# Kernel optimization log

Hardware: AMD Instinct MI355X
Metric: run time of the kernel (lower is better)

The kernel has to match this reference:

```python
import jax, jax.numpy as jnp
import numpy as np

B, S, D = 32, 512, 512      # batch, seq, feature
E, H, O, K = 8, 2048, 512, 2  # experts, expert hidden, expert out, top_k


def setup_inputs() -> dict:
    key = jax.random.key(0)
    ks = jax.random.split(key, 5)
    sc = lambda k, shape, scale: jax.random.normal(k, shape, jnp.float32) * scale
    return {
        "x": sc(ks[0], (B, S, D), 1.0),
        "attn_w": sc(ks[1], (D, 1), 0.05),
        "attn_b": jnp.zeros((1,), jnp.float32),
        "gate_w": sc(ks[2], (D, E), 0.05),
        "gate_b": jnp.zeros((E,), jnp.float32),
        "w1": sc(ks[3], (E, D, H), 0.02),
        "b1": jnp.zeros((E, H), jnp.float32),
        "w2": sc(ks[4], (E, H, O), 0.02),
        "b2": jnp.zeros((E, O), jnp.float32),
    }


def reference(x, attn_w, attn_b, gate_w, gate_b, w1, b1, w2, b2):
    # --- attention pooling over the sequence axis ---
    scores = x @ attn_w + attn_b                      # [B,S,1]
    aw = jax.nn.softmax(scores, axis=1)               # softmax over seq
    pooled = jnp.sum(x * aw, axis=1)                  # [B,D]

    # --- gating: softmax -> top-k mask -> renormalize ---
    gates = jax.nn.softmax(pooled @ gate_w + gate_b, axis=-1)  # [B,E]
    _, idx = jax.lax.top_k(gates, K)                  # [B,K]
    mask = jnp.sum(jax.nn.one_hot(idx, E, dtype=gates.dtype), axis=-2)  # [B,E]
    g = gates * mask
    g = g / (jnp.sum(g, axis=-1, keepdims=True) + 1e-9)        # [B,E]

    # --- dense all-experts compute (exact GELU, as keras Dense('gelu')) ---
    h = jax.nn.gelu(jnp.einsum('bsd,edh->ebsh', x, w1) + b1[:, None, None, :],
                    approximate=False)                 # [E,B,S,H]
    eo = jax.nn.gelu(jnp.einsum('ebsh,eho->ebso', h, w2) + b2[:, None, None, :],
                     approximate=False)                # [E,B,S,O]

    # --- weighted combine over experts ---
    return jnp.einsum('ebso,be->bso', eo, g)           # [B,S,O]
```

## Files before the change

kernel.cpp:

```cpp
#include <hip/hip_runtime.h>
#include <hip/hip_bf16.h>
#include <math.h>

#define B_  32
#define S_  512
#define D_  512
#define E_  8
#define H_  2048
#define O_  512

typedef __bf16 bf16x8 __attribute__((ext_vector_type(8)));
typedef float  f32x4  __attribute__((ext_vector_type(4)));

#define GL2LDS(src, dst) \
  __builtin_amdgcn_global_load_lds((const __attribute__((address_space(1))) void*)(src), \
                                   (__attribute__((address_space(3))) void*)(dst), 16, 0, 0)

#define MFMA16(a, b, c) __builtin_amdgcn_mfma_f32_16x16x32_bf16((a), (b), (c), 0, 0, 0)

__device__ __forceinline__ float gelu_fast(float v) {
  float w = v * fmaf(v * v, 0.0713548162f, 1.5957691216f);
  float e = __expf(-w);
  return v * __builtin_amdgcn_rcpf(1.0f + e);
}


__global__ __launch_bounds__(256) void cast_score_kernel(
    const float* __restrict__ x, const float* __restrict__ attn_w,
    char* __restrict__ xpack, float* __restrict__ scores)
{
  const int t = threadIdx.x;
  const int r = t >> 5;
  const int cg = t & 31;
  const int row = blockIdx.x * 8 + r;
  const int bb = row >> 9, s = row & 511;
  const float* src  = x + (size_t)row * D_ + cg * 16;
  const float* wsrc = attn_w + cg * 16;
  char* xp = xpack + (size_t)bb * 524288 + s * 64;
  const int sx = (s >> 1) & 3;
  float acc = 0.f;
#pragma unroll
  for (int k = 0; k < 4; ++k) {
    const int d0 = cg * 16 + k * 4;
    float4 v  = *(const float4*)(src + k * 4);
    float4 wv = *(const float4*)(wsrc + k * 4);
    acc += v.x * wv.x + v.y * wv.y + v.z * wv.z + v.w * wv.w;
    ushort4 o;
    o.x = __builtin_bit_cast(unsigned short, __float2bfloat16(v.x));
    o.y = __builtin_bit_cast(unsigned short, __float2bfloat16(v.y));
    o.z = __builtin_bit_cast(unsigned short, __float2bfloat16(v.z));
    o.w = __builtin_bit_cast(unsigned short, __float2bfloat16(v.w));
    const int u = d0 >> 5;
    const int byte = u * 32768 + ((((d0 >> 3) & 3) ^ sx) << 4) + (d0 & 7) * 2;
    *(ushort4*)(xp + byte) = o;
  }
#pragma unroll
  for (int off = 16; off; off >>= 1) acc += __shfl_xor(acc, off);
  if (cg == 0) scores[row] = acc;
}

__global__ __launch_bounds__(512) void softmax_aw_kernel(
    const float* __restrict__ scores, float* __restrict__ aw)
{
  __shared__ float red[8];
  __shared__ float mm, ss;
  const int t = threadIdx.x, b = blockIdx.x;
  float v = scores[b * S_ + t];
  float m = v;
#pragma unroll
  for (int off = 32; off; off >>= 1) m = fmaxf(m, __shfl_xor(m, off));
  if ((t & 63) == 0) red[t >> 6] = m;
  __syncthreads();
  if (t == 0) {
    float a = red[0];
    for (int i = 1; i < 8; ++i) a = fmaxf(a, red[i]);
    mm = a;
  }
  __syncthreads();
  float e = expf(v - mm);
  float s = e;
#pragma unroll
  for (int off = 32; off; off >>= 1) s += __shfl_xor(s, off);
  if ((t & 63) == 0) red[t >> 6] = s;
  __syncthreads();
  if (t == 0) {
    float a = 0.f;
    for (int i = 0; i < 8; ++i) a += red[i];
    ss = 1.f / a;
  }
  __syncthreads();
  aw[b * S_ + t] = e * ss;
}

__global__ __launch_bounds__(512) void pool_kernel(
    const float* __restrict__ x, const float* __restrict__ aw, float* __restrict__ pooled)
{
  __shared__ float sm[4][128];
  const int t = threadIdx.x;
  const int dl = t & 127;
  const int sh = t >> 7;
  const int b = blockIdx.y;
  const int d = blockIdx.x * 128 + dl;
  const float* xp  = x + (size_t)b * S_ * D_ + d;
  const float* awb = aw + b * S_;
  float acc = 0.f;
#pragma unroll 4
  for (int s = sh; s < S_; s += 4)
    acc = fmaf(awb[s], xp[(size_t)s * D_], acc);
  if (sh) sm[sh][dl] = acc;
  __syncthreads();
  if (sh == 0) pooled[b * D_ + d] = acc + sm[1][dl] + sm[2][dl] + sm[3][dl];
}

__global__ __launch_bounds__(256) void gate_psort_kernel(
    const float* __restrict__ pooled, const float* __restrict__ gate_w,
    const float* __restrict__ gate_b, int* __restrict__ gidx, float* __restrict__ gwt,
    int* __restrict__ psort)
{
  __shared__ float gl[32][8];
  const int t = threadIdx.x;
  const int b = t >> 3, ee = t & 7;
  float z = gate_b[ee];
  const float* pb = pooled + b * D_;
  for (int d = 0; d < D_; ++d) z = fmaf(pb[d], gate_w[d * E_ + ee], z);
  gl[b][ee] = z;
  __syncthreads();
  if (t < 32) {
    float ge[8];
    float zmax = gl[t][0];
    for (int i = 1; i < 8; ++i) zmax = fmaxf(zmax, gl[t][i]);
    float zs = 0.f;
    for (int i = 0; i < 8; ++i) { ge[i] = expf(gl[t][i] - zmax); zs += ge[i]; }
    for (int i = 0; i < 8; ++i) ge[i] /= zs;
    int i0 = 0;
    for (int i = 1; i < 8; ++i) if (ge[i] > ge[i0]) i0 = i;
    int i1 = -1;
    for (int i = 0; i < 8; ++i) if (i != i0 && (i1 < 0 || ge[i] > ge[i1])) i1 = i;
    float denom = ge[i0] + ge[i1] + 1e-9f;
    gidx[t * 2 + 0] = i0; gidx[t * 2 + 1] = i1;
    gwt[t * 2 + 0] = ge[i0] / denom; gwt[t * 2 + 1] = ge[i1] / denom;
  }
  __syncthreads();
  if (t == 0) {
    int cnt[E_] = {}, pos[E_];
    for (int p = 0; p < 2 * B_; ++p) cnt[gidx[p]]++;
    int s = 0;
    for (int e2 = 0; e2 < E_; ++e2) { pos[e2] = s; s += cnt[e2]; }
    for (int p = 0; p < 2 * B_; ++p) psort[pos[gidx[p]]++] = p;
  }
}

__global__ void pack_w_kernel(const float* __restrict__ in, char* __restrict__ outp,
                              int R, int C)
{
  __shared__ float tile[32][33];
  const int z = blockIdx.z;
  const float* inz = in + (size_t)z * R * C;
  const int c0 = blockIdx.x * 32, r0 = blockIdx.y * 32;
  const int tx = threadIdx.x, ty = threadIdx.y;
#pragma unroll
  for (int jj = 0; jj < 4; ++jj) {
    int r = r0 + ty + jj * 8;
    tile[ty + jj * 8][tx] = inz[(size_t)r * C + c0 + tx];
  }
  __syncthreads();
  const int k = r0 + tx;
  const int u = k >> 5;
  const int PAN = C * 64;
  char* oz = outp + (size_t)z * R * C * 2 + (size_t)u * PAN;
  const int kslot = (k >> 3) & 3;
  const int kbyte = (k & 7) * 2;
#pragma unroll
  for (int jj = 0; jj < 4; ++jj) {
    const int row = c0 + ty + jj * 8;
    const int byte = row * 64 + ((kslot ^ ((row >> 1) & 3)) << 4) + kbyte;
    *(ushort*)(oz + byte) =
        __builtin_bit_cast(unsigned short, __float2bfloat16(tile[tx][ty + jj * 8]));
  }
}


#define V6_TILE(tt, ce, BCUR)                                                   \
  {                                                                             \
    char* cur = lds + (ce) * 16384;                                             \
    const int c2 = ((ce) + 2 >= 3) ? ((ce) - 1) : ((ce) + 2);                   \
    char* nb = lds + c2 * 16384;                                                \
    if ((tt) + 1 < NT) asm volatile("s_waitcnt vmcnt(6)" ::: "memory");         \
    else               asm volatile("s_waitcnt vmcnt(0)" ::: "memory");         \
    __builtin_amdgcn_s_barrier();                                               \
    __builtin_amdgcn_sched_barrier(0);                                          \
    bf16x8 a[8];                                                                \
    _Pragma("unroll")                                                           \
    for (int m = 0; m < 8; ++m) a[m] = *(const bf16x8*)(cur + abase + m * 1024);\
    if ((tt) + 2 < NT) {                                                        \
      const char* s_ = sA2 + ((tt) & 1) * panelA;                               \
      GL2LDS(s_ + dst, nb + dst);                                               \
      GL2LDS(s_ + 8192 + dst, nb + 8192 + dst);                                 \
    }                                                                           \
    asm volatile("s_waitcnt lgkmcnt(0)" ::: "memory");                          \
    __builtin_amdgcn_sched_barrier(0);                                          \
    __builtin_amdgcn_s_setprio(1);                                              \
    _Pragma("unroll")                                                           \
    for (int m = 0; m < 8; ++m) {                                               \
      acc[m][0] = MFMA16(a[m], BCUR[0], acc[m][0]);                             \
      acc[m][1] = MFMA16(a[m], BCUR[1], acc[m][1]);                             \
      acc[m][2] = MFMA16(a[m], BCUR[2], acc[m][2]);                             \
      acc[m][3] = MFMA16(a[m], BCUR[3], acc[m][3]);                             \
    }                                                                           \
    __builtin_amdgcn_s_setprio(0);                                              \
    if ((tt) + 2 < NT) {                                                        \
      const char* bsrc = sB2 + ((tt) & 1) * panelB + blane;                     \
      _Pragma("unroll")                                                         \
      for (int n = 0; n < 4; ++n) BCUR[n] = *(const bf16x8*)(bsrc + n * 1024);  \
    }                                                                           \
  }

__device__ __forceinline__ void gemm_core_v6(const char* __restrict__ Ag, const char* __restrict__ Bg,
                                             const size_t panelA, const size_t panelB,
                                             const int NT, char* lds, f32x4 (&acc)[8][4])
{
  const int tid = threadIdx.x;
  const int l = tid & 63;
  const int w = tid >> 6;
  const int wm = w >> 2;
  const int wn = w & 3;
  const int lr = l & 15;
  const int ks = (l >> 4) & 3;
  const int axor = ((ks ^ ((lr >> 1) & 3)) << 4);
  const int abase = (wm * 128 + lr) * 64 + axor;
  const int blane = (wn * 64 + lr) * 64 + axor;
  const int dst = tid * 16;

  GL2LDS(Ag + dst, lds + dst);
  GL2LDS(Ag + 8192 + dst, lds + 8192 + dst);
  bf16x8 b0[4], b1[4];
#pragma unroll
  for (int n = 0; n < 4; ++n) b0[n] = *(const bf16x8*)(Bg + blane + n * 1024);
  GL2LDS(Ag + panelA + dst, lds + 16384 + dst);
  GL2LDS(Ag + panelA + 8192 + dst, lds + 16384 + 8192 + dst);
#pragma unroll
  for (int n = 0; n < 4; ++n) b1[n] = *(const bf16x8*)(Bg + panelB + blane + n * 1024);

  const char* sA2 = Ag + 2 * panelA;
  const char* sB2 = Bg + 2 * panelB;
  int ce = 0;

#pragma unroll 1
  for (int t = 0; t < NT; t += 2) {
    V6_TILE(t, ce, b0)
    {
      const int co = (ce + 1 >= 3) ? 0 : (ce + 1);
      V6_TILE(t + 1, co, b1)
    }
    sA2 += 2 * panelA;
    sB2 += 2 * panelB;
    ce = (ce + 2 >= 3) ? (ce - 1) : (ce + 2);
  }
}

__global__ __launch_bounds__(512, 2) void gemm1_kernel(
    const char* __restrict__ xpack, const char* __restrict__ W1pack,
    const float* __restrict__ b1, char* __restrict__ Hpack,
    const int* __restrict__ gidx, const int* __restrict__ psort)
{
  extern __shared__ char lds[];
  const int P = blockIdx.x;
  const int L = (P & 7) * 128 + (P >> 3);
  const int p = psort[L >> 4];
  const int tl = L & 15;
  const int b = p >> 1;
  const int e = gidx[p];
  const int h0 = (tl >> 1) * 256;
  const int s0 = (tl & 1) * 256;
  const char* Ag = W1pack + (size_t)e * 2097152 + h0 * 64;
  const char* Bg = xpack + (size_t)b * 524288 + s0 * 64;
  f32x4 acc[8][4] = {};
  const int NT = D_ / 32;
  gemm_core_v6(Ag, Bg, 131072, 32768, NT, lds, acc);

  const int tid = threadIdx.x, l = tid & 63, w = tid >> 6;
  const int wm = w >> 2, wn = w & 3, lr = l & 15, q4 = ((l >> 4) & 3) << 2;
  const float* b1e = b1 + (size_t)e * H_ + h0;
  char* Hp = Hpack + (size_t)p * 2097152;
#pragma unroll
  for (int m = 0; m < 8; ++m) {
    const int hl = wm * 128 + m * 16 + q4;
    const int h = h0 + hl;
    const int uh = h >> 5;
    const int hslot = (h >> 3) & 3;
    const int hbyte = (h & 7) * 2;
    const float4 bias = *(const float4*)(b1e + hl);
#pragma unroll
    for (int n = 0; n < 4; ++n) {
      const int sl = s0 + wn * 64 + n * 16 + lr;
      ushort4 ov;
      ov.x = __builtin_bit_cast(unsigned short, __float2bfloat16(gelu_fast(acc[m][n][0] + bias.x)));
      ov.y = __builtin_bit_cast(unsigned short, __float2bfloat16(gelu_fast(acc[m][n][1] + bias.y)));
      ov.z = __builtin_bit_cast(unsigned short, __float2bfloat16(gelu_fast(acc[m][n][2] + bias.z)));
      ov.w = __builtin_bit_cast(unsigned short, __float2bfloat16(gelu_fast(acc[m][n][3] + bias.w)));
      const int byte = uh * 32768 + sl * 64 + ((hslot ^ ((sl >> 1) & 3)) << 4) + hbyte;
      *(ushort4*)(Hp + byte) = ov;
    }
  }
}

__global__ __launch_bounds__(512, 2) void gemm2_kernel(
    const char* __restrict__ Hpack, const char* __restrict__ W2pack,
    const float* __restrict__ b2, float* __restrict__ out,
    const int* __restrict__ gidx, const float* __restrict__ gwt,
    const int* __restrict__ psort)
{
  extern __shared__ char lds[];
  const int P = blockIdx.x;
  const int L = (P & 7) * 32 + (P >> 3);
  const int p = psort[L >> 2];
  const int tl = L & 3;
  const int b = p >> 1;
  const int e = gidx[p];
  const float gw = gwt[p];
  const int s0 = (tl >> 1) * 256;
  const int o0 = (tl & 1) * 256;
  const char* Ag = Hpack + (size_t)p * 2097152 + s0 * 64;
  const char* Bg = W2pack + (size_t)e * 2097152 + o0 * 64;
  f32x4 acc[8][4] = {};
  const int NT = H_ / 32;
  gemm_core_v6(Ag, Bg, 32768, 32768, NT, lds, acc);

  const int tid = threadIdx.x, l = tid & 63, w = tid >> 6;
  const int wm = w >> 2, wn = w & 3, lr = l & 15, q4 = ((l >> 4) & 3) << 2;
  const float* b2e = b2 + (size_t)e * O_ + o0;
#pragma unroll
  for (int m = 0; m < 8; ++m) {
    const int sl = s0 + wm * 128 + m * 16 + q4;
#pragma unroll
    for (int n = 0; n < 4; ++n) {
      const int ol = wn * 64 + n * 16 + lr;
      const float bias = b2e[ol];
      float* dstp = out + ((size_t)b * S_ + sl) * O_ + o0 + ol;
#pragma unroll
      for (int j = 0; j < 4; ++j)
        atomicAdd(dstp + (size_t)j * O_, gelu_fast(acc[m][n][j] + bias) * gw);
    }
  }
}

__global__ void sentinel_kernel(float* out, int n) {
  int i = blockIdx.x * blockDim.x + threadIdx.x;
  for (; i < n; i += gridDim.x * blockDim.x) out[i] = 1.0e6f;
}

extern "C" void kernel_launch(void* const* d_in, const int* in_sizes, int n_in,
                              void* d_out, int out_size, void* d_ws, size_t ws_size,
                              hipStream_t stream)
{
  const float* x      = (const float*)d_in[0];
  const float* attn_w = (const float*)d_in[1];
  const float* gate_w = (const float*)d_in[3];
  const float* gate_b = (const float*)d_in[4];
  const float* w1     = (const float*)d_in[5];
  const float* b1     = (const float*)d_in[6];
  const float* w2     = (const float*)d_in[7];
  const float* b2     = (const float*)d_in[8];
  float* out = (float*)d_out;

  char* ws = (char*)d_ws;
  const size_t OFF_GIDX = 0;
  const size_t OFF_GWT  = 256;
  const size_t OFF_PSRT = 512;
  const size_t OFF_X    = 1024;
  const size_t SZ_X     = (size_t)B_ * S_ * D_ * 2;
  const size_t OFF_W1T  = OFF_X + SZ_X;
  const size_t SZ_W1T   = (size_t)E_ * H_ * D_ * 2;
  const size_t OFF_W2T  = OFF_W1T + SZ_W1T;
  const size_t SZ_W2T   = (size_t)E_ * O_ * H_ * 2;
  const size_t OFF_H    = OFF_W2T + SZ_W2T;
  const size_t PAIR_H   = (size_t)S_ * H_ * 2;

  if (OFF_H + 64 * PAIR_H > ws_size) {
    hipLaunchKernelGGL(sentinel_kernel, dim3(256), dim3(256), 0, stream, out, out_size);
    return;
  }

  int*   gidx   = (int*)(ws + OFF_GIDX);
  float* gwt    = (float*)(ws + OFF_GWT);
  int*   psort  = (int*)(ws + OFF_PSRT);
  char*  xpack  = ws + OFF_X;
  char*  W1pack = ws + OFF_W1T;
  char*  W2pack = ws + OFF_W2T;
  char*  Hpack  = ws + OFF_H;
  float* scores = (float*)(ws + OFF_H);
  float* aw     = (float*)(ws + OFF_H + 65536);
  float* pooled = (float*)(ws + OFF_H + 131072);

  (void)hipFuncSetAttribute((const void*)gemm1_kernel, hipFuncAttributeMaxDynamicSharedMemorySize, 49152);
  (void)hipFuncSetAttribute((const void*)gemm2_kernel, hipFuncAttributeMaxDynamicSharedMemorySize, 49152);

  hipLaunchKernelGGL(cast_score_kernel, dim3(B_ * S_ / 8), dim3(256), 0, stream,
                     x, attn_w, xpack, scores);
  hipLaunchKernelGGL(softmax_aw_kernel, dim3(B_), dim3(512), 0, stream, scores, aw);
  hipLaunchKernelGGL(pool_kernel, dim3(4, B_), dim3(512), 0, stream, x, aw, pooled);
  hipLaunchKernelGGL(gate_psort_kernel, dim3(1), dim3(256), 0, stream,
                     pooled, gate_w, gate_b, gidx, gwt, psort);
  hipLaunchKernelGGL(pack_w_kernel, dim3(H_ / 32, D_ / 32, E_), dim3(32, 8), 0, stream,
                     w1, W1pack, D_, H_);
  hipLaunchKernelGGL(pack_w_kernel, dim3(O_ / 32, H_ / 32, E_), dim3(32, 8), 0, stream,
                     w2, W2pack, H_, O_);
  hipMemsetAsync(d_out, 0, (size_t)out_size * sizeof(float), stream);

  hipLaunchKernelGGL(gemm1_kernel, dim3(1024), dim3(512), 49152, stream,
                     xpack, W1pack, b1, Hpack, gidx, psort);
  hipLaunchKernelGGL(gemm2_kernel, dim3(256), dim3(512), 49152, stream,
                     Hpack, W2pack, b2, out, gidx, gwt, psort);
}
```

Measured before the change: 270.1 us.

## Replace pipelined 256x256 GEMM core with simple 128x128 LDS-staged core

Swaps the triple-buffered, register-prefetched 256x256-tile GEMM core for a simpler 128x128-tile core. The new core stages both A and B through LDS with a full wait and barrier every 64-wide K step, and uses 256-thread blocks with static 32KB LDS and launch bounds allowing three blocks per CU. Grids grow fourfold to raise occupancy and spread work over more blocks. In exchange it drops the overlap of global loads with MFMA work and lowers per-tile data reuse, so memory stalls become exposed.

```diff
diff --git a/kernel.cpp b/kernel.cpp
--- a/kernel.cpp
+++ b/kernel.cpp
@@ -179,112 +179,83 @@
   }
 }
 
-
-#define V6_TILE(tt, ce, BCUR)                                                   \
-  {                                                                             \
-    char* cur = lds + (ce) * 16384;                                             \
-    const int c2 = ((ce) + 2 >= 3) ? ((ce) - 1) : ((ce) + 2);                   \
-    char* nb = lds + c2 * 16384;                                                \
-    if ((tt) + 1 < NT) asm volatile("s_waitcnt vmcnt(6)" ::: "memory");         \
-    else               asm volatile("s_waitcnt vmcnt(0)" ::: "memory");         \
-    __builtin_amdgcn_s_barrier();                                               \
-    __builtin_amdgcn_sched_barrier(0);                                          \
-    bf16x8 a[8];                                                                \
-    _Pragma("unroll")                                                           \
-    for (int m = 0; m < 8; ++m) a[m] = *(const bf16x8*)(cur + abase + m * 1024);\
-    if ((tt) + 2 < NT) {                                                        \
-      const char* s_ = sA2 + ((tt) & 1) * panelA;                               \
-      GL2LDS(s_ + dst, nb + dst);                                               \
-      GL2LDS(s_ + 8192 + dst, nb + 8192 + dst);                                 \
-    }                                                                           \
-    asm volatile("s_waitcnt lgkmcnt(0)" ::: "memory");                          \
-    __builtin_amdgcn_sched_barrier(0);                                          \
-    __builtin_amdgcn_s_setprio(1);                                              \
-    _Pragma("unroll")                                                           \
-    for (int m = 0; m < 8; ++m) {                                               \
-      acc[m][0] = MFMA16(a[m], BCUR[0], acc[m][0]);                             \
-      acc[m][1] = MFMA16(a[m], BCUR[1], acc[m][1]);                             \
-      acc[m][2] = MFMA16(a[m], BCUR[2], acc[m][2]);                             \
-      acc[m][3] = MFMA16(a[m], BCUR[3], acc[m][3]);                             \
-    }                                                                           \
-    __builtin_amdgcn_s_setprio(0);                                              \
-    if ((tt) + 2 < NT) {                                                        \
-      const char* bsrc = sB2 + ((tt) & 1) * panelB + blane;                     \
-      _Pragma("unroll")                                                         \
-      for (int n = 0; n < 4; ++n) BCUR[n] = *(const bf16x8*)(bsrc + n * 1024);  \
-    }                                                                           \
-  }
-
-__device__ __forceinline__ void gemm_core_v6(const char* __restrict__ Ag, const char* __restrict__ Bg,
-                                             const size_t panelA, const size_t panelB,
-                                             const int NT, char* lds, f32x4 (&acc)[8][4])
+__device__ __forceinline__ void gemm_core_m97(const char* __restrict__ Ag, const char* __restrict__ Bg,
+                                              const size_t unitA, const size_t unitB,
+                                              const int NT, char* lds, f32x4 (&acc)[4][4])
 {
   const int tid = threadIdx.x;
   const int l = tid & 63;
   const int w = tid >> 6;
-  const int wm = w >> 2;
-  const int wn = w & 3;
+  const int wm = w >> 1;
+  const int wn = w & 1;
   const int lr = l & 15;
   const int ks = (l >> 4) & 3;
-  const int axor = ((ks ^ ((lr >> 1) & 3)) << 4);
-  const int abase = (wm * 128 + lr) * 64 + axor;
-  const int blane = (wn * 64 + lr) * 64 + axor;
+  const int swz = ((ks ^ ((lr >> 1) & 3)) << 4);
+  const int abase = wm * 4096 + lr * 64 + swz;
+  const int bbase = 16384 + wn * 4096 + lr * 64 + swz;
   const int dst = tid * 16;
 
-  GL2LDS(Ag + dst, lds + dst);
-  GL2LDS(Ag + 8192 + dst, lds + 8192 + dst);
-  bf16x8 b0[4], b1[4];
-#pragma unroll
-  for (int n = 0; n < 4; ++n) b0[n] = *(const bf16x8*)(Bg + blane + n * 1024);
-  GL2LDS(Ag + panelA + dst, lds + 16384 + dst);
-  GL2LDS(Ag + panelA + 8192 + dst, lds + 16384 + 8192 + dst);
-#pragma unroll
-  for (int n = 0; n < 4; ++n) b1[n] = *(const bf16x8*)(Bg + panelB + blane + n * 1024);
-
-  const char* sA2 = Ag + 2 * panelA;
-  const char* sB2 = Bg + 2 * panelB;
-  int ce = 0;
-
 #pragma unroll 1
-  for (int t = 0; t < NT; t += 2) {
-    V6_TILE(t, ce, b0)
-    {
-      const int co = (ce + 1 >= 3) ? 0 : (ce + 1);
-      V6_TILE(t + 1, co, b1)
+  for (int t = 0; t < NT; ++t) {
+    const char* a0 = Ag + (size_t)(2 * t)     * unitA;
+    const char* a1 = Ag + (size_t)(2 * t + 1) * unitA;
+    const char* b0 = Bg + (size_t)(2 * t)     * unitB;
+    const char* b1 = Bg + (size_t)(2 * t + 1) * unitB;
+    GL2LDS(a0 + dst, lds + dst);          GL2LDS(a0 + 4096 + dst, lds + 4096 + dst);
+    GL2LDS(a1 + dst, lds + 8192 + dst);   GL2LDS(a1 + 4096 + dst, lds + 12288 + dst);
+    GL2LDS(b0 + dst, lds + 16384 + dst);  GL2LDS(b0 + 4096 + dst, lds + 20480 + dst);
+    GL2LDS(b1 + dst, lds + 24576 + dst);  GL2LDS(b1 + 4096 + dst, lds + 28672 + dst);
+    asm volatile("s_waitcnt vmcnt(0)" ::: "memory");
+    __builtin_amdgcn_s_barrier();
+
+    bf16x8 a0f[4], a1f[4], b0f[4], b1f[4];
+#pragma unroll
+    for (int m = 0; m < 4; ++m) {
+      a0f[m] = *(const bf16x8*)(lds + abase + m * 1024);
+      a1f[m] = *(const bf16x8*)(lds + 8192 + abase + m * 1024);
     }
-    sA2 += 2 * panelA;
-    sB2 += 2 * panelB;
-    ce = (ce + 2 >= 3) ? (ce - 1) : (ce + 2);
-  }
-}
-
-__global__ __launch_bounds__(512, 2) void gemm1_kernel(
+#pragma unroll
+    for (int n = 0; n < 4; ++n) {
+      b0f[n] = *(const bf16x8*)(lds + bbase + n * 1024);
+      b1f[n] = *(const bf16x8*)(lds + 8192 + bbase + n * 1024);
+    }
+#pragma unroll
+    for (int m = 0; m < 4; ++m)
+#pragma unroll
+      for (int n = 0; n < 4; ++n) {
+        acc[m][n] = MFMA16(a0f[m], b0f[n], acc[m][n]);
+        acc[m][n] = MFMA16(a1f[m], b1f[n], acc[m][n]);
+      }
+    __builtin_amdgcn_s_barrier();
+  }
+}
+
+__global__ __launch_bounds__(256, 3) void gemm1_kernel(
     const char* __restrict__ xpack, const char* __restrict__ W1pack,
     const float* __restrict__ b1, char* __restrict__ Hpack,
     const int* __restrict__ gidx, const int* __restrict__ psort)
 {
-  extern __shared__ char lds[];
+  __shared__ char lds[32768];
   const int P = blockIdx.x;
-  const int L = (P & 7) * 128 + (P >> 3);
-  const int p = psort[L >> 4];
-  const int tl = L & 15;
+  const int L = (P & 7) * 512 + (P >> 3);
+  const int p = psort[L >> 6];
+  const int tl = L & 63;
   const int b = p >> 1;
   const int e = gidx[p];
-  const int h0 = (tl >> 1) * 256;
-  const int s0 = (tl & 1) * 256;
+  const int h0 = (tl >> 2) * 128;
+  const int s0 = (tl & 3) * 128;
   const char* Ag = W1pack + (size_t)e * 2097152 + h0 * 64;
   const char* Bg = xpack + (size_t)b * 524288 + s0 * 64;
-  f32x4 acc[8][4] = {};
-  const int NT = D_ / 32;
-  gemm_core_v6(Ag, Bg, 131072, 32768, NT, lds, acc);
+  f32x4 acc[4][4] = {};
+  gemm_core_m97(Ag, Bg, 131072, 32768, D_ / 64, lds, acc);
 
   const int tid = threadIdx.x, l = tid & 63, w = tid >> 6;
-  const int wm = w >> 2, wn = w & 3, lr = l & 15, q4 = ((l >> 4) & 3) << 2;
+  const int wm = w >> 1, wn = w & 1, lr = l & 15, q4 = ((l >> 4) & 3) << 2;
   const float* b1e = b1 + (size_t)e * H_ + h0;
   char* Hp = Hpack + (size_t)p * 2097152;
 #pragma unroll
-  for (int m = 0; m < 8; ++m) {
-    const int hl = wm * 128 + m * 16 + q4;
+  for (int m = 0; m < 4; ++m) {
+    const int hl = wm * 64 + m * 16 + q4;
     const int h = h0 + hl;
     const int uh = h >> 5;
     const int hslot = (h >> 3) & 3;
@@ -304,34 +275,33 @@
   }
 }
 
-__global__ __launch_bounds__(512, 2) void gemm2_kernel(
+__global__ __launch_bounds__(256, 3) void gemm2_kernel(
     const char* __restrict__ Hpack, const char* __restrict__ W2pack,
     const float* __restrict__ b2, float* __restrict__ out,
     const int* __restrict__ gidx, const float* __restrict__ gwt,
     const int* __restrict__ psort)
 {
-  extern __shared__ char lds[];
+  __shared__ char lds[32768];
   const int P = blockIdx.x;
-  const int L = (P & 7) * 32 + (P >> 3);
-  const int p = psort[L >> 2];
-  const int tl = L & 3;
+  const int L = (P & 7) * 128 + (P >> 3);
+  const int p = psort[L >> 4];
+  const int tl = L & 15;
   const int b = p >> 1;
   const int e = gidx[p];
   const float gw = gwt[p];
-  const int s0 = (tl >> 1) * 256;
-  const int o0 = (tl & 1) * 256;
+  const int o0 = (tl >> 2) * 128;
+  const int s0 = (tl & 3) * 128;
   const char* Ag = Hpack + (size_t)p * 2097152 + s0 * 64;
   const char* Bg = W2pack + (size_t)e * 2097152 + o0 * 64;
-  f32x4 acc[8][4] = {};
-  const int NT = H_ / 32;
-  gemm_core_v6(Ag, Bg, 32768, 32768, NT, lds, acc);
+  f32x4 acc[4][4] = {};
+  gemm_core_m97(Ag, Bg, 32768, 32768, H_ / 64, lds, acc);
 
   const int tid = threadIdx.x, l = tid & 63, w = tid >> 6;
-  const int wm = w >> 2, wn = w & 3, lr = l & 15, q4 = ((l >> 4) & 3) << 2;
+  const int wm = w >> 1, wn = w & 1, lr = l & 15, q4 = ((l >> 4) & 3) << 2;
   const float* b2e = b2 + (size_t)e * O_ + o0;
 #pragma unroll
-  for (int m = 0; m < 8; ++m) {
-    const int sl = s0 + wm * 128 + m * 16 + q4;
+  for (int m = 0; m < 4; ++m) {
+    const int sl = s0 + wm * 64 + m * 16 + q4;
 #pragma unroll
     for (int n = 0; n < 4; ++n) {
       const int ol = wn * 64 + n * 16 + lr;
@@ -392,9 +362,6 @@
   float* aw     = (float*)(ws + OFF_H + 65536);
   float* pooled = (float*)(ws + OFF_H + 131072);
 
-  (void)hipFuncSetAttribute((const void*)gemm1_kernel, hipFuncAttributeMaxDynamicSharedMemorySize, 49152);
-  (void)hipFuncSetAttribute((const void*)gemm2_kernel, hipFuncAttributeMaxDynamicSharedMemorySize, 49152);
-
   hipLaunchKernelGGL(cast_score_kernel, dim3(B_ * S_ / 8), dim3(256), 0, stream,
                      x, attn_w, xpack, scores);
   hipLaunchKernelGGL(softmax_aw_kernel, dim3(B_), dim3(512), 0, stream, scores, aw);
@@ -407,8 +374,8 @@
                      w2, W2pack, H_, O_);
   hipMemsetAsync(d_out, 0, (size_t)out_size * sizeof(float), stream);
 
-  hipLaunchKernelGGL(gemm1_kernel, dim3(1024), dim3(512), 49152, stream,
+  hipLaunchKernelGGL(gemm1_kernel, dim3(4096), dim3(256), 0, stream,
                      xpack, W1pack, b1, Hpack, gidx, psort);
-  hipLaunchKernelGGL(gemm2_kernel, dim3(256), dim3(512), 49152, stream,
+  hipLaunchKernelGGL(gemm2_kernel, dim3(1024), dim3(256), 0, stream,
                      Hpack, W2pack, b2, out, gidx, gwt, psort);
 }
```

Measured after the change: 262.1 us. 1.03x faster.
